# Kernel optimization log

Measured on AMD Instinct MI355X. Metric: run time of the kernel, lower is better.

Reference implementation:

```python
import jax, jax.numpy as jnp
import numpy as np

DT = 0.1
B_SZ = 8192
T_HIST = 20
LEN_PRED = 30
FEAT = 32
N_LAYERS = 3
# state transition for constant-acceleration model (matches self.F in torch)
F_MAT = np.array([[1.0, DT, DT * DT / 2], [0.0, 1.0, DT], [0.0, 0.0, 1.0]], dtype=np.float32)


def setup_inputs() -> dict:
    key = jax.random.key(0)
    ks = jax.random.split(key, 16)
    # random-walk trajectories as history observations
    hist = jnp.cumsum(jax.random.normal(ks[0], (B_SZ, T_HIST, 2), jnp.float32) * 0.5, axis=1)
    k_lin = 1.0 / np.sqrt(FEAT)
    k_in = 1.0 / np.sqrt(24)

    def u(k, shape, scale):
        return jax.random.uniform(k, shape, jnp.float32, -scale, scale)

    return {
        "hist": hist,
        "max_accel_x": jnp.ones((1,), jnp.float32) * 10.0,
        "max_accel_y": jnp.ones((1,), jnp.float32) * 20.0,
        "velocity_std_x": jnp.ones((1,), jnp.float32) * 10.0,
        "acceleration_std_x": jnp.ones((1,), jnp.float32) * 10.0,
        "R_x_": jnp.array([0.0448], jnp.float32),
        "R_y_": jnp.array([0.001], jnp.float32),
        "G_x": jnp.array([0.0059, 0.2981, 0.0393], jnp.float32),
        "G_y": jnp.array([0.0059, 0.2981, 0.0393], jnp.float32) / 5.0,
        "Win_W": u(ks[1], (FEAT, 24), k_in),
        "Win_b": u(ks[2], (FEAT,), k_in),
        "enc_Wih": u(ks[3], (N_LAYERS, 4 * FEAT, FEAT), k_lin),
        "enc_Whh": u(ks[4], (N_LAYERS, 4 * FEAT, FEAT), k_lin),
        "enc_bih": u(ks[5], (N_LAYERS, 4 * FEAT), k_lin),
        "enc_bhh": u(ks[6], (N_LAYERS, 4 * FEAT), k_lin),
        "dec_Wih": u(ks[7], (N_LAYERS, 4 * FEAT, FEAT), k_lin),
        "dec_Whh": u(ks[8], (N_LAYERS, 4 * FEAT, FEAT), k_lin),
        "dec_bih": u(ks[9], (N_LAYERS, 4 * FEAT), k_lin),
        "dec_bhh": u(ks[10], (N_LAYERS, 4 * FEAT), k_lin),
        "Wout_W": u(ks[11], (4, FEAT), k_lin),
        "Wout_b": u(ks[12], (4,), k_lin),
        "len_pred": LEN_PRED,
    }


def reference(hist, max_accel_x, max_accel_y, velocity_std_x, acceleration_std_x,
              R_x_, R_y_, G_x, G_y, Win_W, Win_b,
              enc_Wih, enc_Whh, enc_bih, enc_bhh,
              dec_Wih, dec_Whh, dec_bih, dec_bhh,
              Wout_W, Wout_b, len_pred):
    B = hist.shape[0]
    F = jnp.asarray(F_MAT)
    R_x = R_x_[0] * R_x_[0]
    R_y = R_y_[0] * R_y_[0]
    Z_x = hist[:, :, 0]
    Z_y = hist[:, :, 1]

    def lstm(x, h, c, Wih, Whh, bih, bhh):
        g = x @ Wih.T + bih + h @ Whh.T + bhh
        i, f, gg, o = jnp.split(g, 4, axis=1)
        c = jax.nn.sigmoid(f) * c + jax.nn.sigmoid(i) * jnp.tanh(gg)
        h = jax.nn.sigmoid(o) * jnp.tanh(c)
        return h, c

    def stack(XP, h, c, Wih, Whh, bih, bhh):
        x = jnp.tanh(XP @ Win_W.T + Win_b)
        hs, cs = [], []
        for j in range(N_LAYERS):
            hj, cj = lstm(x, h[j], c[j], Wih[j], Whh[j], bih[j], bhh[j])
            hs.append(hj)
            cs.append(cj)
            x = cj  # torch code feeds the fresh CELL state to the next layer
        return jnp.stack(hs), jnp.stack(cs)

    def kpred(X, P, Q):
        return X @ F.T, jnp.einsum('ij,bjk,lk->bil', F, P, F) + Q

    def kupdate(X, P, z, R):
        y = z - X[:, 0]                      # innovation (H picks component 0)
        S = P[:, 0, 0] + R                   # innovation covariance (scalar)
        K = P[:, :, 0] / S[:, None]          # Kalman gain (B,3)
        return X + y[:, None] * K, P - K[:, :, None] * P[:, 0:1, :]

    def kinit(z0):
        # torch always calls _kalman_init with is_x=True (default), so both
        # axes use R_x / velocity_std_x / acceleration_std_x
        X = jnp.zeros((B, 3), hist.dtype).at[:, 0].set(z0)
        d = jnp.stack([R_x, velocity_std_x[0] ** 2, acceleration_std_x[0] ** 2])
        P = jnp.zeros((B, 3, 3), hist.dtype).at[:, jnp.arange(3), jnp.arange(3)].set(d)
        return X, P

    Qx_e = jnp.outer(G_x * max_accel_x[0], G_x * max_accel_x[0])
    Qy_e = jnp.outer(G_y * max_accel_y[0], G_y * max_accel_y[0])

    Xx, Px = kinit(Z_x[:, 0])
    Xy, Py = kinit(Z_y[:, 0])
    h = jnp.zeros((N_LAYERS, B, FEAT), hist.dtype)
    c = jnp.zeros_like(h)

    def enc_step(carry, zs):
        Xx, Px, Xy, Py, h, c = carry
        zx, zy = zs
        XP = jnp.concatenate([Xx, Xy, Px.reshape(B, 9), Py.reshape(B, 9)], 1)
        h, c = stack(XP, h, c, enc_Wih, enc_Whh, enc_bih, enc_bhh)
        Xx, Px = kpred(Xx, Px, Qx_e)
        Xy, Py = kpred(Xy, Py, Qy_e)
        Xx, Px = kupdate(Xx, Px, zx, R_x)
        Xy, Py = kupdate(Xy, Py, zy, R_y)
        return (Xx, Px, Xy, Py, h, c), None

    carry, _ = jax.lax.scan(enc_step, (Xx, Px, Xy, Py, h, c),
                            (Z_x[:, 1:].T, Z_y[:, 1:].T))

    oxx = jnp.outer(G_x, G_x)
    oyy = jnp.outer(G_y, G_y)

    def dec_step(carry, _):
        Xx, Px, Xy, Py, h, c = carry
        XP = jnp.concatenate([Xx, Xy, Px.reshape(B, 9), Py.reshape(B, 9)], 1)
        h, c = stack(XP, h, c, dec_Wih, dec_Whh, dec_bih, dec_bhh)
        pred = c[-1] @ Wout_W.T + Wout_b  # (B,4): [u_x, u_y, std_x, std_y]
        Xx = Xx.at[:, 2].set(DT * pred[:, 0])  # X[:,2] = B*u
        Xy = Xy.at[:, 2].set(DT * pred[:, 1])
        Qx = (pred[:, 2] ** 2)[:, None, None] * oxx
        Qy = (pred[:, 3] ** 2)[:, None, None] * oyy
        Xx, Px = kpred(Xx, Px, Qx)
        Xy, Py = kpred(Xy, Py, Qy)
        out = jnp.stack([Xx[:, 0], Xy[:, 0],
                         jnp.sqrt(Px[:, 0, 0]), jnp.sqrt(Py[:, 0, 0]),
                         jnp.zeros(B, hist.dtype)], axis=1)  # (B,5)
        return (Xx, Px, Xy, Py, h, c), out

    carry, ys = jax.lax.scan(dec_step, carry, None, length=len_pred)
    return jnp.transpose(ys, (1, 0, 2))  # (B, len_pred, 5)
```

## Files before the change

kernel.cpp:

```cpp
#include <hip/hip_runtime.h>
#include <math.h>

#define DT   0.1f
#define HDT  0.005f
#define T_HIST 20
#define LEN_PRED 30

typedef __attribute__((ext_vector_type(8))) short bfrag8;
typedef __attribute__((ext_vector_type(4))) float f32x4;
typedef __attribute__((ext_vector_type(2))) unsigned int u32x2;

#define WS_FRAG   0u
#define WS_WIN    98304u
#define WS_WOUT   100352u
#define WS_BIAS   101376u

static __device__ __forceinline__ unsigned short f2bf(float x) {
    union { float f; unsigned int u; } v; v.f = x;
    unsigned int r = v.u + 0x7fffu + ((v.u >> 16) & 1u);
    return (unsigned short)(r >> 16);
}

static __device__ __forceinline__ unsigned int cvtpk(float lo, float hi) {
    unsigned int r;
    asm("v_cvt_pk_bf16_f32 %0, %1, %2" : "=v"(r) : "v"(lo), "v"(hi));
    return r;
}

__global__ void prep_kernel(const float* __restrict__ Win_W,
                            const float* __restrict__ eWih, const float* __restrict__ eWhh,
                            const float* __restrict__ ebih, const float* __restrict__ ebhh,
                            const float* __restrict__ dWih, const float* __restrict__ dWhh,
                            const float* __restrict__ dbih, const float* __restrict__ dbhh,
                            const float* __restrict__ Wout_W,
                            char* __restrict__ ws)
{
    int i = blockIdx.x * blockDim.x + threadIdx.x;
    if (i < 49152) {
        int fi = i >> 9, within = i & 511;
        int lane = within >> 3, jj = within & 7;
        int t = fi & 7, c = (fi >> 3) & 1;
        int pl = fi >> 4;
        int l = pl % 3, ph = pl / 3;
        int p = lane & 15, q2 = lane >> 4;
        int gate = p & 3;
        int feat = (t >> 1) * 8 + 2 * (p >> 2) + (t & 1);
        int row = gate * 32 + feat;
        int k = q2 * 8 + jj;
        const float* W = (c == 0) ? (ph ? dWih : eWih) : (ph ? dWhh : eWhh);
        ((unsigned short*)(ws + WS_FRAG))[i] = f2bf(W[l * 4096 + row * 32 + k]);
    } else if (i < 50176) {
        int i2 = i - 49152;
        int w = i2 >> 9, within = i2 & 511;
        int lane = within >> 3, jj = within & 7;
        int p = lane & 15, q2 = lane >> 4;
        int k = q2 * 8 + jj;
        float v = (k < 24) ? Win_W[(w * 16 + p) * 24 + k] : 0.f;
        ((unsigned short*)(ws + WS_WIN))[i2] = f2bf(v);
    } else if (i < 50688) {
        int i3 = i - 50176;
        int lane = i3 >> 3, jj = i3 & 7;
        int p = lane & 15, q2 = lane >> 4;
        float v = Wout_W[(p & 3) * 32 + q2 * 8 + jj];
        ((unsigned short*)(ws + WS_WOUT))[i3] = f2bf(v);
    } else if (i < 51456) {
        int b = i - 50688;
        int ph = b / 384, rem = b % 384;
        int l = rem >> 7, w2 = rem & 127;
        int col = w2 >> 2, r = w2 & 3;
        const float* bi = ph ? dbih : ebih;
        const float* bh = ph ? dbhh : ebhh;
        ((float*)(ws + WS_BIAS))[b] = bi[l * 128 + r * 32 + col] + bh[l * 128 + r * 32 + col];
    }
}

__launch_bounds__(512, 4)
__global__ void kalman_lstm_kernel(const float* __restrict__ hist,
                                   const float* __restrict__ max_ax, const float* __restrict__ max_ay,
                                   const float* __restrict__ vstd, const float* __restrict__ astd,
                                   const float* __restrict__ Rx_, const float* __restrict__ Ry_,
                                   const float* __restrict__ Gx, const float* __restrict__ Gy,
                                   const float* __restrict__ Win_b, const float* __restrict__ Wout_b,
                                   const char* __restrict__ ws, float* __restrict__ out)
{
    __shared__ __align__(16) unsigned int xchC[3][2][4][16][4];
    __shared__ __align__(16) unsigned int xchH[3][2][4][16][4];
    __shared__ __align__(16) unsigned int xenc[T_HIST - 1][4][16][4];
    __shared__ __align__(16) unsigned int x0b[4][16][4];

    const int tid  = threadIdx.x;
    const int wv   = tid >> 6;
    const int lane = tid & 63;
    const int q    = lane >> 4;
    const int m    = lane & 15;
    const int be   = blockIdx.x * 16 + m;
    const f32x4 zero4 = {0.f, 0.f, 0.f, 0.f};

    const bfrag8* fragp = (const bfrag8*)(ws + WS_FRAG);
    const f32x4*  biasp = (const f32x4*)(ws + WS_BIAS);

    bfrag8 fragA[3][2];
    f32x4  biasV[3];
    auto load_phase = [&](int ph) {
#pragma unroll
        for (int l = 0; l < 3; ++l) {
#pragma unroll
            for (int c = 0; c < 2; ++c)
                fragA[l][c] = fragp[(((ph * 3 + l) * 2 + c) * 8 + wv) * 64 + lane];
            biasV[l] = biasp[ph * 96 + l * 32 + ((wv >> 1) * 8 + 2 * q + (wv & 1))];
        }
    };
    load_phase(0);

    const int w = (wv >= 6) ? (wv - 6) : 0;
    bfrag8 winF = ((const bfrag8*)(ws + WS_WIN))[w * 64 + lane];
    f32x4 winBv;
#pragma unroll
    for (int r = 0; r < 4; ++r) winBv[r] = Win_b[w * 16 + q * 4 + r];
    bfrag8 woutF = ((const bfrag8*)(ws + WS_WOUT))[lane];
    const float wb0 = Wout_b[0], wb1 = Wout_b[1], wb2 = Wout_b[2], wb3 = Wout_b[3];

    const float rx = Rx_[0] * Rx_[0], ry = Ry_[0] * Ry_[0];
    const float gX0 = Gx[0], gX1 = Gx[1], gX2 = Gx[2];
    const float gY0 = Gy[0], gY1 = Gy[1], gY2 = Gy[2];
    const float gx00 = gX0*gX0, gx01 = gX0*gX1, gx02 = gX0*gX2,
                gx11 = gX1*gX1, gx12 = gX1*gX2, gx22 = gX2*gX2;
    const float gy00 = gY0*gY0, gy01 = gY0*gY1, gy02 = gY0*gY2,
                gy11 = gY1*gY1, gy12 = gY1*gY2, gy22 = gY2*gY2;
    const float sx2 = max_ax[0] * max_ax[0], sy2 = max_ay[0] * max_ay[0];
    const float ex00 = gx00*sx2, ex01 = gx01*sx2, ex02 = gx02*sx2,
                ex11 = gx11*sx2, ex12 = gx12*sx2, ex22 = gx22*sx2;
    const float ey00 = gy00*sy2, ey01 = gy01*sy2, ey02 = gy02*sy2,
                ey11 = gy11*sy2, ey12 = gy12*sy2, ey22 = gy22*sy2;
    const float pv = vstd[0] * vstd[0], pa = astd[0] * astd[0];

    float Xx0 = hist[be * 40 + 0], Xx1 = 0.f, Xx2 = 0.f;
    float Xy0 = hist[be * 40 + 1], Xy1 = 0.f, Xy2 = 0.f;
    float Px00 = rx, Px01 = 0.f, Px02 = 0.f, Px11 = pv, Px12 = 0.f, Px22 = pa;
    float Py00 = rx, Py01 = 0.f, Py02 = 0.f, Py11 = pv, Py12 = 0.f, Py22 = pa;

    float creg[3] = {0.f, 0.f, 0.f};

    auto sig = [](float z) { return __builtin_amdgcn_rcpf(1.f + __expf(-z)); };
    auto th  = [](float z) { return fmaf(-2.f, __builtin_amdgcn_rcpf(__expf(2.f * z) + 1.f), 1.f); };

    auto kpred9 = [](float& X0, float& X1, float& X2,
                     float& P00, float& P01, float& P02, float& P11, float& P12, float& P22,
                     float Q00, float Q01, float Q02, float Q11, float Q12, float Q22) {
        X0 = X0 + DT * X1 + HDT * X2;
        X1 = X1 + DT * X2;
        float M00 = P00 + DT * P01 + HDT * P02;
        float M01 = P01 + DT * P11 + HDT * P12;
        float M02 = P02 + DT * P12 + HDT * P22;
        float M11 = P11 + DT * P12;
        float M12 = P12 + DT * P22;
        float M22 = P22;
        P00 = M00 + DT * M01 + HDT * M02 + Q00;
        P01 = M01 + DT * M02 + Q01;
        P02 = M02 + Q02;
        P11 = M11 + DT * M12 + Q11;
        P12 = M12 + Q12;
        P22 = M22 + Q22;
    };
    auto kupd9 = [](float& X0, float& X1, float& X2,
                    float& P00, float& P01, float& P02, float& P11, float& P12, float& P22,
                    float z, float R) {
        float y = z - X0;
        float Sinv = 1.0f / (P00 + R);
        float K0 = P00 * Sinv, K1 = P01 * Sinv, K2 = P02 * Sinv;
        X0 += y * K0; X1 += y * K1; X2 += y * K2;
        float p00 = P00, p01 = P01, p02 = P02;
        P00 = p00 - K0 * p00;
        P01 = p01 - K0 * p01;
        P02 = p02 - K0 * p02;
        P11 = P11 - K1 * p01;
        P12 = P12 - K1 * p02;
        P22 = P22 - K2 * p02;
    };
    auto kf_enc_step = [&](int s) {
        float zx = hist[be * 40 + s * 2], zy = hist[be * 40 + s * 2 + 1];
        kpred9(Xx0, Xx1, Xx2, Px00, Px01, Px02, Px11, Px12, Px22, ex00, ex01, ex02, ex11, ex12, ex22);
        kupd9 (Xx0, Xx1, Xx2, Px00, Px01, Px02, Px11, Px12, Px22, zx, rx);
        kpred9(Xy0, Xy1, Xy2, Py00, Py01, Py02, Py11, Py12, Py22, ey00, ey01, ey02, ey11, ey12, ey22);
        kupd9 (Xy0, Xy1, Xy2, Py00, Py01, Py02, Py11, Py12, Py22, zy, ry);
    };

    auto packf = [&](const float* v) {
        union { bfrag8 f; unsigned int u[4]; } u;
#pragma unroll
        for (int d = 0; d < 4; ++d) u.u[d] = cvtpk(v[2 * d], v[2 * d + 1]);
        return u.f;
    };
    auto build_xp = [&]() {
        float v[8];
        if (q == 0)      { v[0]=Xx0;  v[1]=Xx1;  v[2]=Xx2;  v[3]=Xy0;  v[4]=Xy1;  v[5]=Xy2;  v[6]=Px00; v[7]=Px01; }
        else if (q == 1) { v[0]=Px02; v[1]=Px01; v[2]=Px11; v[3]=Px12; v[4]=Px02; v[5]=Px12; v[6]=Px22; v[7]=Py00; }
        else if (q == 2) { v[0]=Py01; v[1]=Py02; v[2]=Py01; v[3]=Py11; v[4]=Py12; v[5]=Py02; v[6]=Py12; v[7]=Py22; }
        else             { v[0]=0.f; v[1]=0.f; v[2]=0.f; v[3]=0.f; v[4]=0.f; v[5]=0.f; v[6]=0.f; v[7]=0.f; }
        return packf(v);
    };
    auto win_emit = [&](unsigned int* dst) {
        bfrag8 xpf = build_xp();
        f32x4 aw = __builtin_amdgcn_mfma_f32_16x16x32_bf16(winF, xpf, winBv, 0, 0, 0);
        u32x2 pk;
        pk.x = cvtpk(th(aw[0]), th(aw[1]));
        pk.y = cvtpk(th(aw[2]), th(aw[3]));
        *(u32x2*)(dst + ((2 * w + (q >> 1)) * 16 + m) * 4 + (q & 1) * 2) = pk;
    };

    const int sidx = ((wv >> 1) * 16 + m) * 8 + 2 * q + (wv & 1);
    auto cell = [&](int l, bfrag8 xf, bfrag8 hf, unsigned int* Cb, unsigned int* Hb) {
        f32x4 a = __builtin_amdgcn_mfma_f32_16x16x32_bf16(fragA[l][1], hf, biasV[l], 0, 0, 0);
        a = __builtin_amdgcn_mfma_f32_16x16x32_bf16(fragA[l][0], xf, a, 0, 0, 0);
        float iv = sig(a[0]), fv = sig(a[1]), gv = th(a[2]), ov = sig(a[3]);
        float c = fmaf(fv, creg[l], iv * gv);
        creg[l] = c;
        float h = ov * th(c);
        unsigned int pk = cvtpk(c, h);
        ((unsigned short*)Cb)[sidx] = (unsigned short)pk;
        ((unsigned short*)Hb)[sidx] = (unsigned short)(pk >> 16);
    };

    bfrag8 c2f = bfrag8{};
    auto do_pred = [&](int tout) {
        f32x4 ap = __builtin_amdgcn_mfma_f32_16x16x32_bf16(woutF, c2f, zero4, 0, 0, 0);
        float p0 = ap[0] + wb0, p1 = ap[1] + wb1, p2 = ap[2] + wb2, p3 = ap[3] + wb3;
        Xx2 = DT * p0; Xy2 = DT * p1;
        float qsx = p2 * p2, qsy = p3 * p3;
        kpred9(Xx0, Xx1, Xx2, Px00, Px01, Px02, Px11, Px12, Px22,
               qsx*gx00, qsx*gx01, qsx*gx02, qsx*gx11, qsx*gx12, qsx*gx22);
        kpred9(Xy0, Xy1, Xy2, Py00, Py01, Py02, Py11, Py12, Py22,
               qsy*gy00, qsy*gy01, qsy*gy02, qsy*gy11, qsy*gy12, qsy*gy22);
        if (wv == 6 && q == 0) {
            float* o = out + (size_t)be * (LEN_PRED * 5) + tout * 5;
            o[0] = Xx0; o[1] = Xy0; o[2] = sqrtf(Px00); o[3] = sqrtf(Py00); o[4] = 0.f;
        }
    };

    for (int i = tid; i < 3 * 2 * 4 * 16 * 4; i += 512) {
        (&xchC[0][0][0][0][0])[i] = 0;
        (&xchH[0][0][0][0][0])[i] = 0;
    }

    if (wv >= 6) {
#pragma unroll 1
        for (int s = 0; s < T_HIST - 1; ++s) {
            if (s > 0) kf_enc_step(s);
            win_emit(&xenc[s][0][0][0]);
        }
        kf_enc_step(T_HIST - 1);
    }
    __syncthreads();

#pragma unroll 1
    for (int p = 0; p < T_HIST + 1; ++p) {
        const int pw = p & 1, pr = pw ^ 1;
        if (p <= T_HIST - 2) {
            bfrag8 xf = *(const bfrag8*)&xenc[p][q][m][0];
            bfrag8 hf = *(const bfrag8*)&xchH[0][pr][q][m][0];
            cell(0, xf, hf, &xchC[0][pw][0][0][0], &xchH[0][pw][0][0][0]);
        }
        if (p >= 1 && p <= T_HIST - 1) {
            bfrag8 xf = *(const bfrag8*)&xchC[0][pr][q][m][0];
            bfrag8 hf = *(const bfrag8*)&xchH[1][pr][q][m][0];
            cell(1, xf, hf, &xchC[1][pw][0][0][0], &xchH[1][pw][0][0][0]);
        }
        if (p >= 2) {
            bfrag8 xf = *(const bfrag8*)&xchC[1][pr][q][m][0];
            bfrag8 hf = *(const bfrag8*)&xchH[2][pr][q][m][0];
            cell(2, xf, hf, &xchC[2][pw][0][0][0], &xchH[2][pw][0][0][0]);
        }
        __syncthreads();
    }

    load_phase(1);
    bfrag8 hfragR[3];
    hfragR[0] = *(const bfrag8*)&xchH[0][0][q][m][0];
    hfragR[1] = *(const bfrag8*)&xchH[1][1][q][m][0];
    hfragR[2] = *(const bfrag8*)&xchH[2][0][q][m][0];
    c2f       = *(const bfrag8*)&xchC[2][0][q][m][0];

#pragma unroll 1
    for (int t = 0; t < LEN_PRED; ++t) {
        f32x4 ah[3];
#pragma unroll
        for (int l = 0; l < 3; ++l)
            ah[l] = __builtin_amdgcn_mfma_f32_16x16x32_bf16(fragA[l][1], hfragR[l], biasV[l], 0, 0, 0);

        if (wv >= 6) {
            if (t > 0) do_pred(t - 1);
            win_emit(&x0b[0][0][0]);
        }
        __syncthreads();

        bfrag8 xf = *(const bfrag8*)&x0b[q][m][0];
#pragma unroll
        for (int l = 0; l < 3; ++l) {
            f32x4 a = __builtin_amdgcn_mfma_f32_16x16x32_bf16(fragA[l][0], xf, ah[l], 0, 0, 0);
            float iv = sig(a[0]), fv = sig(a[1]), gv = th(a[2]), ov = sig(a[3]);
            float c = fmaf(fv, creg[l], iv * gv);
            creg[l] = c;
            float h = ov * th(c);
            unsigned int pk = cvtpk(c, h);
            ((unsigned short*)&xchC[l][0][0][0][0])[sidx] = (unsigned short)pk;
            ((unsigned short*)&xchH[l][0][0][0][0])[sidx] = (unsigned short)(pk >> 16);
            __syncthreads();
            xf        = *(const bfrag8*)&xchC[l][0][q][m][0];
            hfragR[l] = *(const bfrag8*)&xchH[l][0][q][m][0];
        }
        c2f = xf;
    }
    if (wv >= 6) do_pred(LEN_PRED - 1);
}

extern "C" void kernel_launch(void* const* d_in, const int* in_sizes, int n_in,
                              void* d_out, int out_size, void* d_ws, size_t ws_size,
                              hipStream_t stream)
{
    const float* hist  = (const float*)d_in[0];
    const float* maxax = (const float*)d_in[1];
    const float* maxay = (const float*)d_in[2];
    const float* vstd  = (const float*)d_in[3];
    const float* astd  = (const float*)d_in[4];
    const float* Rx    = (const float*)d_in[5];
    const float* Ry    = (const float*)d_in[6];
    const float* Gx    = (const float*)d_in[7];
    const float* Gy    = (const float*)d_in[8];
    const float* WinW  = (const float*)d_in[9];
    const float* Winb  = (const float*)d_in[10];
    const float* eWih  = (const float*)d_in[11];
    const float* eWhh  = (const float*)d_in[12];
    const float* ebih  = (const float*)d_in[13];
    const float* ebhh  = (const float*)d_in[14];
    const float* dWih  = (const float*)d_in[15];
    const float* dWhh  = (const float*)d_in[16];
    const float* dbih  = (const float*)d_in[17];
    const float* dbhh  = (const float*)d_in[18];
    const float* WoutW = (const float*)d_in[19];
    const float* Woutb = (const float*)d_in[20];
    char* ws = (char*)d_ws;
    float* out = (float*)d_out;

    prep_kernel<<<202, 256, 0, stream>>>(WinW, eWih, eWhh, ebih, ebhh,
                                         dWih, dWhh, dbih, dbhh, WoutW, ws);
    kalman_lstm_kernel<<<512, 512, 0, stream>>>(hist, maxax, maxay, vstd, astd,
                                                Rx, Ry, Gx, Gy, Winb, Woutb,
                                                ws, out);
}
```

Baseline: 197.4 us.

## Halve block to 4 waves with two gate tiles per wave and pipelined encoder KF

The block shrinks from 8 to 4 waves. Each wave now computes two 16-column gate tiles per LSTM layer, which doubles its MFMA and gate work and halves the block-wide barrier participants. The Kalman-filter encoder step and input projection are moved inside the layered pipeline loop with a double-buffered xenc, replacing the serial pre-pass. This shortens the critical-path prologue and LDS footprint, at the cost of more per-wave serial work and higher register pressure from the duplicated fragments.

Result: faster. 189.5 us (-4.0%).

```diff
diff --git a/kernel.cpp b/kernel.cpp
--- a/kernel.cpp
+++ b/kernel.cpp
@@ -74,7 +74,7 @@
     }
 }
 
-__launch_bounds__(512, 4)
+__launch_bounds__(256, 2)
 __global__ void kalman_lstm_kernel(const float* __restrict__ hist,
                                    const float* __restrict__ max_ax, const float* __restrict__ max_ay,
                                    const float* __restrict__ vstd, const float* __restrict__ astd,
@@ -85,7 +85,7 @@
 {
     __shared__ __align__(16) unsigned int xchC[3][2][4][16][4];
     __shared__ __align__(16) unsigned int xchH[3][2][4][16][4];
-    __shared__ __align__(16) unsigned int xenc[T_HIST - 1][4][16][4];
+    __shared__ __align__(16) unsigned int xenc[2][4][16][4];
     __shared__ __align__(16) unsigned int x0b[4][16][4];
 
     const int tid  = threadIdx.x;
@@ -99,20 +99,24 @@
     const bfrag8* fragp = (const bfrag8*)(ws + WS_FRAG);
     const f32x4*  biasp = (const f32x4*)(ws + WS_BIAS);
 
-    bfrag8 fragA[3][2];
-    f32x4  biasV[3];
+    bfrag8 fragA[3][2][2];
+    f32x4  biasV[3][2];
     auto load_phase = [&](int ph) {
 #pragma unroll
         for (int l = 0; l < 3; ++l) {
 #pragma unroll
             for (int c = 0; c < 2; ++c)
-                fragA[l][c] = fragp[(((ph * 3 + l) * 2 + c) * 8 + wv) * 64 + lane];
-            biasV[l] = biasp[ph * 96 + l * 32 + ((wv >> 1) * 8 + 2 * q + (wv & 1))];
+#pragma unroll
+                for (int j = 0; j < 2; ++j)
+                    fragA[l][c][j] = fragp[(((ph * 3 + l) * 2 + c) * 8 + (2 * wv + j)) * 64 + lane];
+#pragma unroll
+            for (int j = 0; j < 2; ++j)
+                biasV[l][j] = biasp[ph * 96 + l * 32 + (wv * 8 + 2 * q + j)];
         }
     };
     load_phase(0);
 
-    const int w = (wv >= 6) ? (wv - 6) : 0;
+    const int w = (wv >= 2) ? (wv - 2) : 0;
     bfrag8 winF = ((const bfrag8*)(ws + WS_WIN))[w * 64 + lane];
     f32x4 winBv;
 #pragma unroll
@@ -134,12 +138,20 @@
                 ey11 = gy11*sy2, ey12 = gy12*sy2, ey22 = gy22*sy2;
     const float pv = vstd[0] * vstd[0], pa = astd[0] * astd[0];
 
-    float Xx0 = hist[be * 40 + 0], Xx1 = 0.f, Xx2 = 0.f;
-    float Xy0 = hist[be * 40 + 1], Xy1 = 0.f, Xy2 = 0.f;
-    float Px00 = rx, Px01 = 0.f, Px02 = 0.f, Px11 = pv, Px12 = 0.f, Px22 = pa;
-    float Py00 = rx, Py01 = 0.f, Py02 = 0.f, Py11 = pv, Py12 = 0.f, Py22 = pa;
-
-    float creg[3] = {0.f, 0.f, 0.f};
+    float Xx0 = 0.f, Xx1 = 0.f, Xx2 = 0.f;
+    float Xy0 = 0.f, Xy1 = 0.f, Xy2 = 0.f;
+    float Px00 = 0.f, Px01 = 0.f, Px02 = 0.f, Px11 = 0.f, Px12 = 0.f, Px22 = 0.f;
+    float Py00 = 0.f, Py01 = 0.f, Py02 = 0.f, Py11 = 0.f, Py12 = 0.f, Py22 = 0.f;
+    if (wv >= 2) {
+        Xx0 = hist[be * 40 + 0];
+        Xy0 = hist[be * 40 + 1];
+        Px00 = rx; Px11 = pv; Px22 = pa;
+        Py00 = rx; Py11 = pv; Py22 = pa;
+    }
+
+    float creg[3][2];
+#pragma unroll
+    for (int l = 0; l < 3; ++l) { creg[l][0] = 0.f; creg[l][1] = 0.f; }
 
     auto sig = [](float z) { return __builtin_amdgcn_rcpf(1.f + __expf(-z)); };
     auto th  = [](float z) { return fmaf(-2.f, __builtin_amdgcn_rcpf(__expf(2.f * z) + 1.f), 1.f); };
@@ -208,20 +220,80 @@
         *(u32x2*)(dst + ((2 * w + (q >> 1)) * 16 + m) * 4 + (q & 1) * 2) = pk;
     };
 
-    const int sidx = ((wv >> 1) * 16 + m) * 8 + 2 * q + (wv & 1);
-    auto cell = [&](int l, bfrag8 xf, bfrag8 hf, unsigned int* Cb, unsigned int* Hb) {
-        f32x4 a = __builtin_amdgcn_mfma_f32_16x16x32_bf16(fragA[l][1], hf, biasV[l], 0, 0, 0);
-        a = __builtin_amdgcn_mfma_f32_16x16x32_bf16(fragA[l][0], xf, a, 0, 0, 0);
+    auto gates_from = [&](int l, int j, f32x4 a, float& cv, float& hv) {
         float iv = sig(a[0]), fv = sig(a[1]), gv = th(a[2]), ov = sig(a[3]);
-        float c = fmaf(fv, creg[l], iv * gv);
-        creg[l] = c;
-        float h = ov * th(c);
-        unsigned int pk = cvtpk(c, h);
-        ((unsigned short*)Cb)[sidx] = (unsigned short)pk;
-        ((unsigned short*)Hb)[sidx] = (unsigned short)(pk >> 16);
-    };
-
-    bfrag8 c2f = bfrag8{};
+        float c = fmaf(fv, creg[l][j], iv * gv);
+        creg[l][j] = c;
+        cv = c;
+        hv = ov * th(c);
+    };
+
+    for (int i = tid; i < 3 * 2 * 4 * 16 * 4; i += 256) {
+        (&xchC[0][0][0][0][0])[i] = 0;
+        (&xchH[0][0][0][0][0])[i] = 0;
+    }
+
+    if (wv >= 2) win_emit(&xenc[0][0][0][0]);
+    __syncthreads();
+
+#pragma unroll 1
+    for (int p = 0; p < T_HIST + 1; ++p) {
+        const int pw = p & 1, pr = pw ^ 1;
+        if (wv >= 2 && p <= T_HIST - 3) {
+            kf_enc_step(p + 1);
+            win_emit(&xenc[(p + 1) & 1][0][0][0]);
+        }
+        const bool b0 = (p <= T_HIST - 2);
+        const bool b1 = (p >= 1) && (p <= T_HIST - 1);
+        const bool b2 = (p >= 2);
+        unsigned int cd0, hd0, cd1, hd1, cd2, hd2;
+        if (b0) {
+            bfrag8 xf = *(const bfrag8*)&xenc[pw][q][m][0];
+            bfrag8 hf = *(const bfrag8*)&xchH[0][pr][q][m][0];
+            f32x4 a = __builtin_amdgcn_mfma_f32_16x16x32_bf16(fragA[0][1][0], hf, biasV[0][0], 0, 0, 0);
+            a = __builtin_amdgcn_mfma_f32_16x16x32_bf16(fragA[0][0][0], xf, a, 0, 0, 0);
+            f32x4 b = __builtin_amdgcn_mfma_f32_16x16x32_bf16(fragA[0][1][1], hf, biasV[0][1], 0, 0, 0);
+            b = __builtin_amdgcn_mfma_f32_16x16x32_bf16(fragA[0][0][1], xf, b, 0, 0, 0);
+            float c0, h0, c1, h1;
+            gates_from(0, 0, a, c0, h0); gates_from(0, 1, b, c1, h1);
+            cd0 = cvtpk(c0, c1); hd0 = cvtpk(h0, h1);
+        }
+        if (b1) {
+            bfrag8 xf = *(const bfrag8*)&xchC[0][pr][q][m][0];
+            bfrag8 hf = *(const bfrag8*)&xchH[1][pr][q][m][0];
+            f32x4 a = __builtin_amdgcn_mfma_f32_16x16x32_bf16(fragA[1][1][0], hf, biasV[1][0], 0, 0, 0);
+            a = __builtin_amdgcn_mfma_f32_16x16x32_bf16(fragA[1][0][0], xf, a, 0, 0, 0);
+            f32x4 b = __builtin_amdgcn_mfma_f32_16x16x32_bf16(fragA[1][1][1], hf, biasV[1][1], 0, 0, 0);
+            b = __builtin_amdgcn_mfma_f32_16x16x32_bf16(fragA[1][0][1], xf, b, 0, 0, 0);
+            float c0, h0, c1, h1;
+            gates_from(1, 0, a, c0, h0); gates_from(1, 1, b, c1, h1);
+            cd1 = cvtpk(c0, c1); hd1 = cvtpk(h0, h1);
+        }
+        if (b2) {
+            bfrag8 xf = *(const bfrag8*)&xchC[1][pr][q][m][0];
+            bfrag8 hf = *(const bfrag8*)&xchH[2][pr][q][m][0];
+            f32x4 a = __builtin_amdgcn_mfma_f32_16x16x32_bf16(fragA[2][1][0], hf, biasV[2][0], 0, 0, 0);
+            a = __builtin_amdgcn_mfma_f32_16x16x32_bf16(fragA[2][0][0], xf, a, 0, 0, 0);
+            f32x4 b = __builtin_amdgcn_mfma_f32_16x16x32_bf16(fragA[2][1][1], hf, biasV[2][1], 0, 0, 0);
+            b = __builtin_amdgcn_mfma_f32_16x16x32_bf16(fragA[2][0][1], xf, b, 0, 0, 0);
+            float c0, h0, c1, h1;
+            gates_from(2, 0, a, c0, h0); gates_from(2, 1, b, c1, h1);
+            cd2 = cvtpk(c0, c1); hd2 = cvtpk(h0, h1);
+        }
+        if (b0) { xchC[0][pw][wv][m][q] = cd0; xchH[0][pw][wv][m][q] = hd0; }
+        if (b1) { xchC[1][pw][wv][m][q] = cd1; xchH[1][pw][wv][m][q] = hd1; }
+        if (b2) { xchC[2][pw][wv][m][q] = cd2; xchH[2][pw][wv][m][q] = hd2; }
+        __syncthreads();
+    }
+    if (wv >= 2) kf_enc_step(T_HIST - 1);
+
+    load_phase(1);
+    bfrag8 hfragR[3];
+    hfragR[0] = *(const bfrag8*)&xchH[0][0][q][m][0];
+    hfragR[1] = *(const bfrag8*)&xchH[1][1][q][m][0];
+    hfragR[2] = *(const bfrag8*)&xchH[2][0][q][m][0];
+    bfrag8 c2f = *(const bfrag8*)&xchC[2][0][q][m][0];
+
     auto do_pred = [&](int tout) {
         f32x4 ap = __builtin_amdgcn_mfma_f32_16x16x32_bf16(woutF, c2f, zero4, 0, 0, 0);
         float p0 = ap[0] + wb0, p1 = ap[1] + wb1, p2 = ap[2] + wb2, p3 = ap[3] + wb3;
@@ -231,63 +303,22 @@
                qsx*gx00, qsx*gx01, qsx*gx02, qsx*gx11, qsx*gx12, qsx*gx22);
         kpred9(Xy0, Xy1, Xy2, Py00, Py01, Py02, Py11, Py12, Py22,
                qsy*gy00, qsy*gy01, qsy*gy02, qsy*gy11, qsy*gy12, qsy*gy22);
-        if (wv == 6 && q == 0) {
+        if (wv == 2 && q == 0) {
             float* o = out + (size_t)be * (LEN_PRED * 5) + tout * 5;
             o[0] = Xx0; o[1] = Xy0; o[2] = sqrtf(Px00); o[3] = sqrtf(Py00); o[4] = 0.f;
         }
     };
 
-    for (int i = tid; i < 3 * 2 * 4 * 16 * 4; i += 512) {
-        (&xchC[0][0][0][0][0])[i] = 0;
-        (&xchH[0][0][0][0][0])[i] = 0;
-    }
-
-    if (wv >= 6) {
-#pragma unroll 1
-        for (int s = 0; s < T_HIST - 1; ++s) {
-            if (s > 0) kf_enc_step(s);
-            win_emit(&xenc[s][0][0][0]);
-        }
-        kf_enc_step(T_HIST - 1);
-    }
-    __syncthreads();
-
-#pragma unroll 1
-    for (int p = 0; p < T_HIST + 1; ++p) {
-        const int pw = p & 1, pr = pw ^ 1;
-        if (p <= T_HIST - 2) {
-            bfrag8 xf = *(const bfrag8*)&xenc[p][q][m][0];
-            bfrag8 hf = *(const bfrag8*)&xchH[0][pr][q][m][0];
-            cell(0, xf, hf, &xchC[0][pw][0][0][0], &xchH[0][pw][0][0][0]);
-        }
-        if (p >= 1 && p <= T_HIST - 1) {
-            bfrag8 xf = *(const bfrag8*)&xchC[0][pr][q][m][0];
-            bfrag8 hf = *(const bfrag8*)&xchH[1][pr][q][m][0];
-            cell(1, xf, hf, &xchC[1][pw][0][0][0], &xchH[1][pw][0][0][0]);
-        }
-        if (p >= 2) {
-            bfrag8 xf = *(const bfrag8*)&xchC[1][pr][q][m][0];
-            bfrag8 hf = *(const bfrag8*)&xchH[2][pr][q][m][0];
-            cell(2, xf, hf, &xchC[2][pw][0][0][0], &xchH[2][pw][0][0][0]);
-        }
-        __syncthreads();
-    }
-
-    load_phase(1);
-    bfrag8 hfragR[3];
-    hfragR[0] = *(const bfrag8*)&xchH[0][0][q][m][0];
-    hfragR[1] = *(const bfrag8*)&xchH[1][1][q][m][0];
-    hfragR[2] = *(const bfrag8*)&xchH[2][0][q][m][0];
-    c2f       = *(const bfrag8*)&xchC[2][0][q][m][0];
-
 #pragma unroll 1
     for (int t = 0; t < LEN_PRED; ++t) {
-        f32x4 ah[3];
+        f32x4 ah[3][2];
 #pragma unroll
         for (int l = 0; l < 3; ++l)
-            ah[l] = __builtin_amdgcn_mfma_f32_16x16x32_bf16(fragA[l][1], hfragR[l], biasV[l], 0, 0, 0);
-
-        if (wv >= 6) {
+#pragma unroll
+            for (int j = 0; j < 2; ++j)
+                ah[l][j] = __builtin_amdgcn_mfma_f32_16x16x32_bf16(fragA[l][1][j], hfragR[l], biasV[l][j], 0, 0, 0);
+
+        if (wv >= 2) {
             if (t > 0) do_pred(t - 1);
             win_emit(&x0b[0][0][0]);
         }
@@ -296,21 +327,20 @@
         bfrag8 xf = *(const bfrag8*)&x0b[q][m][0];
 #pragma unroll
         for (int l = 0; l < 3; ++l) {
-            f32x4 a = __builtin_amdgcn_mfma_f32_16x16x32_bf16(fragA[l][0], xf, ah[l], 0, 0, 0);
-            float iv = sig(a[0]), fv = sig(a[1]), gv = th(a[2]), ov = sig(a[3]);
-            float c = fmaf(fv, creg[l], iv * gv);
-            creg[l] = c;
-            float h = ov * th(c);
-            unsigned int pk = cvtpk(c, h);
-            ((unsigned short*)&xchC[l][0][0][0][0])[sidx] = (unsigned short)pk;
-            ((unsigned short*)&xchH[l][0][0][0][0])[sidx] = (unsigned short)(pk >> 16);
+            f32x4 a0 = __builtin_amdgcn_mfma_f32_16x16x32_bf16(fragA[l][0][0], xf, ah[l][0], 0, 0, 0);
+            f32x4 a1 = __builtin_amdgcn_mfma_f32_16x16x32_bf16(fragA[l][0][1], xf, ah[l][1], 0, 0, 0);
+            float c0, h0, c1, h1;
+            gates_from(l, 0, a0, c0, h0);
+            gates_from(l, 1, a1, c1, h1);
+            xchC[l][0][wv][m][q] = cvtpk(c0, c1);
+            xchH[l][0][wv][m][q] = cvtpk(h0, h1);
             __syncthreads();
             xf        = *(const bfrag8*)&xchC[l][0][q][m][0];
             hfragR[l] = *(const bfrag8*)&xchH[l][0][q][m][0];
         }
         c2f = xf;
     }
-    if (wv >= 6) do_pred(LEN_PRED - 1);
+    if (wv >= 2) do_pred(LEN_PRED - 1);
 }
 
 extern "C" void kernel_launch(void* const* d_in, const int* in_sizes, int n_in,
@@ -343,7 +373,7 @@
 
     prep_kernel<<<202, 256, 0, stream>>>(WinW, eWih, eWhh, ebih, ebhh,
                                          dWih, dWhh, dbih, dbhh, WoutW, ws);
-    kalman_lstm_kernel<<<512, 512, 0, stream>>>(hist, maxax, maxay, vstd, astd,
+    kalman_lstm_kernel<<<512, 256, 0, stream>>>(hist, maxax, maxay, vstd, astd,
                                                 Rx, Ry, Gx, Gy, Winb, Woutb,
                                                 ws, out);
 }
```
